# Kernel tuning notes

Measured on AMD Instinct MI355X. Metric: run time of the kernel, lower is better.

## Reference

```python
import jax, jax.numpy as jnp
import numpy as np

B, S, D, H = 4, 2048, 1024, 16
HD = D // H  # head_dim = 64


def setup_inputs() -> dict:
    key = jax.random.key(0)
    ks = jax.random.split(key, 7)
    sc = 0.02
    return {
        "data": jax.random.normal(ks[0], (B, S, D), jnp.float32),
        "context": jax.random.normal(ks[1], (B, S, D), jnp.float32),
        "Wq": jax.random.normal(ks[2], (D, D), jnp.float32) * sc,
        "bq": jnp.zeros((D,), jnp.float32),
        "Wk": jax.random.normal(ks[3], (D, D), jnp.float32) * sc,
        "bk": jnp.zeros((D,), jnp.float32),
        "Wv": jax.random.normal(ks[4], (D, D), jnp.float32) * sc,
        "bv": jnp.zeros((D,), jnp.float32),
        "Wo": jax.random.normal(ks[5], (D, D), jnp.float32) * sc,
        "bo": jnp.zeros((D,), jnp.float32),
    }


def reference(data, context, Wq, bq, Wk, bk, Wv, bv, Wo, bo):
    # Projections (torch Linear: x @ W.T + b; here W stored as [in, out])
    Q = data @ Wq + bq          # [B,S,D]
    K = context @ Wk + bk
    V = context @ Wv + bv
    # split heads -> [B,H,S,HD]
    Q = Q.reshape(B, S, H, HD).transpose(0, 2, 1, 3)
    K = K.reshape(B, S, H, HD).transpose(0, 2, 1, 3)
    V = V.reshape(B, S, H, HD).transpose(0, 2, 1, 3)
    scale = jnp.sqrt(jnp.asarray(HD, Q.dtype))
    scores = jnp.einsum("bhqd,bhkd->bhqk", Q, K) / scale  # [B,H,S,S]
    causal = jnp.tril(jnp.ones((S, S), bool))              # row >= col
    scores = jnp.where(causal[None, None], scores, jnp.asarray(-jnp.inf, scores.dtype))
    probs = jax.nn.softmax(scores, axis=-1)
    Z = jnp.einsum("bhqk,bhkd->bhqd", probs, V)            # [B,H,S,HD]
    Z = Z.transpose(0, 2, 1, 3).reshape(B, S, D)
    return Z @ Wo + bo
```

## Files before the change

kernel.cpp:

```cpp
#include <hip/hip_runtime.h>

#define B_  4
#define S_  2048
#define D_  1024
#define H_  16
#define HD_ 64
#define M_  (B_*S_)

typedef _Float16 f16;
typedef f16  f16x8 __attribute__((ext_vector_type(8)));
typedef f16  f16x4 __attribute__((ext_vector_type(4)));
typedef float f32x4 __attribute__((ext_vector_type(4)));

__device__ __forceinline__ void gload_lds16(const f16* g, f16* l) {
    __builtin_amdgcn_global_load_lds(
        (const __attribute__((address_space(1))) void*)g,
        (__attribute__((address_space(3))) void*)l, 16, 0, 0);
}

__global__ __launch_bounds__(256) void cvt2_kernel(const float* __restrict__ a,
                                                   const float* __restrict__ c,
                                                   f16* __restrict__ out, int n4each) {
    int i = blockIdx.x * 256 + threadIdx.x;
    const float* src = (i < n4each) ? a : c;
    int j = (i < n4each) ? i : i - n4each;
    f32x4 v = *reinterpret_cast<const f32x4*>(src + (size_t)j * 4);
    *reinterpret_cast<f16x4*>(out + (size_t)i * 4) = __builtin_convertvector(v, f16x4);
}

__global__ __launch_bounds__(256) void transpose_cvt4_kernel(const float* __restrict__ Wq,
                                                             const float* __restrict__ Wk,
                                                             const float* __restrict__ Wv,
                                                             const float* __restrict__ Wo,
                                                             f16* __restrict__ WT) {
    __shared__ float tile[32][33];
    const int z = blockIdx.z;
    const float* W = (z == 0) ? Wq : (z == 1) ? Wk : (z == 2) ? Wv : Wo;
    f16* dst = WT + (size_t)z * D_ * D_;
    const int n0 = blockIdx.x * 32, k0 = blockIdx.y * 32;
    const int tx = threadIdx.x & 31, ty = threadIdx.x >> 5;
#pragma unroll
    for (int j = 0; j < 4; ++j)
        tile[ty + 8 * j][tx] = W[(size_t)(k0 + ty + 8 * j) * D_ + n0 + tx];
    __syncthreads();
#pragma unroll
    for (int j = 0; j < 4; ++j)
        dst[(size_t)(n0 + ty + 8 * j) * D_ + k0 + tx] = (f16)tile[tx][ty + 8 * j];
}

__global__ __launch_bounds__(512, 2) void gemm_qkv8(const f16* __restrict__ Adata,
                                                    const f16* __restrict__ Actx,
                                                    const f16* __restrict__ Wt,
                                                    const float* __restrict__ bq,
                                                    const float* __restrict__ bk,
                                                    const float* __restrict__ bv,
                                                    f16* __restrict__ Qb,
                                                    f16* __restrict__ Kb,
                                                    f16* __restrict__ VtB) {
    extern __shared__ __align__(16) f16 SM[];
    constexpr int K = D_;
    constexpr int NT = K / 64;
    const int id = (int)(blockIdx.y * 12 + blockIdx.x);
    const int work = (id & 7) * 48 + (id >> 3);
    const int wy = work / 12, wx = work - wy * 12;
    const int seg = wx >> 2;
    const f16* __restrict__ A = seg ? Actx : Adata;
    const int m0 = wy * 256, n0 = wx * 256;
    const int tid = (int)threadIdx.x;
    const int w = tid >> 6, l = tid & 63, lr = l & 15, lg = l >> 4;
    const int wr = w >> 2, wc = w & 3;
    const int swx = lr & 7;
    const int srow = tid >> 3;
    const int g16 = (tid & 7) ^ (srow & 7);

    auto stageH = [&](int buf, int kt, int mat, int h) {
        const f16* __restrict__ src = mat ? (Wt + (size_t)(n0 + h * 128) * K)
                                          : (A + (size_t)(m0 + h * 128) * K);
        f16* dst = SM + mat * 32768 + buf * 16384 + h * 8192;
        const int kk0 = kt * 64;
        gload_lds16(src + (size_t)srow * K + kk0 + g16 * 8, dst + w * 512);
        gload_lds16(src + (size_t)(srow + 64) * K + kk0 + g16 * 8, dst + 4096 + w * 512);
    };
    auto LDA = [&](int buf, int m, int kk) -> f16x8 {
        const int gr = m * 32 + wr * 16 + lr;
        return *reinterpret_cast<const f16x8*>(
            SM + buf * 16384 + (gr >> 7) * 8192 + (gr & 127) * 64 + (((kk * 4 + lg) ^ swx) * 8));
    };
    auto LDB = [&](int buf, int n, int kk) -> f16x8 {
        const int gr = n * 64 + wc * 16 + lr;
        return *reinterpret_cast<const f16x8*>(
            SM + 32768 + buf * 16384 + (gr >> 7) * 8192 + (gr & 127) * 64 + (((kk * 4 + lg) ^ swx) * 8));
    };

    f32x4 acc[8][4] = {};
    stageH(0, 0, 0, 0); stageH(0, 0, 1, 0); stageH(0, 0, 1, 1); stageH(0, 0, 0, 1);
    asm volatile("s_waitcnt vmcnt(4)" ::: "memory");
    __builtin_amdgcn_s_barrier();

    for (int t = 0; t < NT; ++t) {
        const int buf = t & 1, nb = buf ^ 1;
        const bool nl = (t + 1 < NT);
        f16x8 a[4][2], b[4][2];
#pragma unroll
        for (int m = 0; m < 4; ++m) { a[m][0] = LDA(buf, m, 0); a[m][1] = LDA(buf, m, 1); }
#pragma unroll
        for (int n = 0; n < 2; ++n) { b[n][0] = LDB(buf, n, 0); b[n][1] = LDB(buf, n, 1); }
        if (nl) { stageH(nb, t + 1, 0, 0); asm volatile("s_waitcnt vmcnt(4)" ::: "memory"); }
        else    { asm volatile("s_waitcnt vmcnt(2)" ::: "memory"); }
        __builtin_amdgcn_s_barrier();
        __builtin_amdgcn_s_setprio(1);
#pragma unroll
        for (int kk = 0; kk < 2; ++kk)
#pragma unroll
            for (int m = 0; m < 4; ++m)
#pragma unroll
                for (int n = 0; n < 2; ++n)
                    acc[m][n] = __builtin_amdgcn_mfma_f32_16x16x32_f16(a[m][kk], b[n][kk], acc[m][n], 0, 0, 0);
        __builtin_amdgcn_s_setprio(0);
        __builtin_amdgcn_s_barrier();
#pragma unroll
        for (int n = 2; n < 4; ++n) { b[n][0] = LDB(buf, n, 0); b[n][1] = LDB(buf, n, 1); }
        if (nl) { stageH(nb, t + 1, 1, 0); asm volatile("s_waitcnt vmcnt(4)" ::: "memory"); }
        else    { asm volatile("s_waitcnt vmcnt(0)" ::: "memory"); }
        __builtin_amdgcn_s_barrier();
        __builtin_amdgcn_s_setprio(1);
#pragma unroll
        for (int kk = 0; kk < 2; ++kk)
#pragma unroll
            for (int m = 0; m < 4; ++m)
#pragma unroll
                for (int n = 2; n < 4; ++n)
                    acc[m][n] = __builtin_amdgcn_mfma_f32_16x16x32_f16(a[m][kk], b[n][kk], acc[m][n], 0, 0, 0);
        __builtin_amdgcn_s_setprio(0);
        __builtin_amdgcn_s_barrier();
#pragma unroll
        for (int m = 0; m < 4; ++m) { a[m][0] = LDA(buf, m + 4, 0); a[m][1] = LDA(buf, m + 4, 1); }
        if (nl) stageH(nb, t + 1, 1, 1);
        __builtin_amdgcn_s_barrier();
        __builtin_amdgcn_s_setprio(1);
#pragma unroll
        for (int kk = 0; kk < 2; ++kk)
#pragma unroll
            for (int m = 0; m < 4; ++m)
#pragma unroll
                for (int n = 2; n < 4; ++n)
                    acc[m + 4][n] = __builtin_amdgcn_mfma_f32_16x16x32_f16(a[m][kk], b[n][kk], acc[m + 4][n], 0, 0, 0);
        __builtin_amdgcn_s_setprio(0);
        __builtin_amdgcn_s_barrier();
        if (nl) { stageH(nb, t + 1, 0, 1); asm volatile("s_waitcnt vmcnt(4)" ::: "memory"); }
        __builtin_amdgcn_s_barrier();
        __builtin_amdgcn_s_setprio(1);
#pragma unroll
        for (int kk = 0; kk < 2; ++kk)
#pragma unroll
            for (int m = 0; m < 4; ++m)
#pragma unroll
                for (int n = 0; n < 2; ++n)
                    acc[m + 4][n] = __builtin_amdgcn_mfma_f32_16x16x32_f16(a[m][kk], b[n][kk], acc[m + 4][n], 0, 0, 0);
        __builtin_amdgcn_s_setprio(0);
        __builtin_amdgcn_s_barrier();
    }
    const float* bias = (seg == 0) ? bq : (seg == 1) ? bk : bv;
#pragma unroll
    for (int n = 0; n < 4; ++n) {
        const int col = n0 + n * 64 + wc * 16 + lr;
        const int lc = col & 1023;
        const float bvv = bias[lc];
#pragma unroll
        for (int m = 0; m < 8; ++m) {
            const int row = m0 + m * 32 + wr * 16 + lg * 4;
            if (seg == 2) {
                const int bb = row >> 11, s0 = row & 2047;
                f16x4 v;
#pragma unroll
                for (int r = 0; r < 4; ++r) v[r] = (f16)(acc[m][n][r] + bvv);
                *reinterpret_cast<f16x4*>(VtB + ((size_t)(bb * D_ + lc)) * S_ + s0) = v;
            } else {
                f16* dst = seg ? Kb : Qb;
#pragma unroll
                for (int r = 0; r < 4; ++r)
                    dst[(size_t)(row + r) * D_ + lc] = (f16)(acc[m][n][r] + bvv);
            }
        }
    }
}

__global__ __launch_bounds__(256, 2) void gemm_out3(const f16* __restrict__ A,
                                                    const f16* __restrict__ Wt,
                                                    const float* __restrict__ bias,
                                                    float* __restrict__ Cout) {
    extern __shared__ __align__(16) f16 SM[];
    constexpr int K = D_;
    constexpr int NT = K / 32;
    const int id = (int)blockIdx.x;
    const int work = (id & 7) * 32 + (id >> 3);
    const int wy = work >> 2, wx = work & 3;
    const int m0 = wy * 128, n0 = wx * 256;
    const int tid = (int)threadIdx.x;
    const int w = tid >> 6, lr = tid & 15, lg = (tid & 63) >> 4;
    const int wr = w >> 1, wc = w & 1;
    const int sw = (lr >> 1) & 3;

    auto stage = [&](int buf, int kt) {
        const int kk0 = kt * 32;
        f16* base = SM + buf * 12288;
#pragma unroll
        for (int j = 0; j < 2; ++j) {
            const int c = j * 256 + tid;
            const int row = c >> 2;
            const int ks = ((c & 3) ^ ((row >> 1) & 3)) * 8;
            gload_lds16(A + (size_t)(m0 + row) * K + kk0 + ks,
                        base + (j * 256 + w * 64) * 8);
        }
#pragma unroll
        for (int j = 0; j < 4; ++j) {
            const int c = j * 256 + tid;
            const int row = c >> 2;
            const int ks = ((c & 3) ^ ((row >> 1) & 3)) * 8;
            gload_lds16(Wt + (size_t)(n0 + row) * K + kk0 + ks,
                        base + 4096 + (j * 256 + w * 64) * 8);
        }
    };
    auto LDA = [&](int buf, int m) -> f16x8 {
        return *reinterpret_cast<const f16x8*>(
            SM + buf * 12288 + (wr * 64 + m * 16 + lr) * 32 + ((lg ^ sw) * 8));
    };
    auto LDB = [&](int buf, int n) -> f16x8 {
        return *reinterpret_cast<const f16x8*>(
            SM + buf * 12288 + 4096 + (wc * 128 + n * 16 + lr) * 32 + ((lg ^ sw) * 8));
    };

    f32x4 acc[4][8] = {};
    stage(0, 0);
    stage(1, 1);
    asm volatile("s_waitcnt vmcnt(6)" ::: "memory");
    __builtin_amdgcn_s_barrier();

    int buf = 0;
    for (int t = 0; t < NT; ++t) {
        if (t + 2 < NT) {
            int nb = buf + 2; if (nb >= 3) nb -= 3;
            stage(nb, t + 2);
        }
        f16x8 a[4], b[8];
#pragma unroll
        for (int m = 0; m < 4; ++m) a[m] = LDA(buf, m);
#pragma unroll
        for (int n = 0; n < 8; ++n) b[n] = LDB(buf, n);
        __builtin_amdgcn_s_setprio(1);
#pragma unroll
        for (int m = 0; m < 4; ++m)
#pragma unroll
            for (int n = 0; n < 8; ++n)
                acc[m][n] = __builtin_amdgcn_mfma_f32_16x16x32_f16(a[m], b[n], acc[m][n], 0, 0, 0);
        __builtin_amdgcn_s_setprio(0);
        if (t + 2 < NT) {
            asm volatile("s_waitcnt vmcnt(6)" ::: "memory");
        } else if (t + 1 < NT) {
            asm volatile("s_waitcnt vmcnt(0)" ::: "memory");
        }
        __builtin_amdgcn_s_barrier();
        if (++buf >= 3) buf = 0;
    }
#pragma unroll
    for (int n = 0; n < 8; ++n) {
        const int col = n0 + wc * 128 + n * 16 + lr;
        const float bvv = bias[col];
#pragma unroll
        for (int m = 0; m < 4; ++m) {
            const int row = m0 + wr * 64 + m * 16 + lg * 4;
#pragma unroll
            for (int r = 0; r < 4; ++r)
                Cout[(size_t)(row + r) * D_ + col] = acc[m][n][r] + bvv;
        }
    }
}

__global__ __launch_bounds__(256, 2) void attn_kernel(const f16* __restrict__ Q,
                                                      const f16* __restrict__ Kg,
                                                      const f16* __restrict__ Vt,
                                                      f16* __restrict__ Z) {
    __shared__ __align__(16) f16 KL[2][64 * 64];
    __shared__ __align__(16) f16 VL[2][64 * 64];
    __shared__ __align__(16) f16 Pl[4][32][72];
    const int h = blockIdx.x, b = blockIdx.y, pp = blockIdx.z;
    const int tid = threadIdx.x, w = tid >> 6, l = tid & 63, lr = l & 15, lg = l >> 4;
    const size_t base   = ((size_t)b * S_) * D_ + h * HD_;
    const size_t vtbase = ((size_t)(b * D_ + h * HD_)) * S_;
    const f16* __restrict__ Kbase = Kg + base;
    const f16* __restrict__ Vbase = Vt + vtbase;
    const float sc = 0.125f * 1.44269504f;
    const int sw_xor = lr & 7;
    f16x8 onesv;
#pragma unroll
    for (int i = 0; i < 8; ++i) onesv[i] = (f16)1.0f;

    auto stageKV = [&](int buf, int t0) {
#pragma unroll
        for (int i = 0; i < 2; ++i) {
            const int c = i * 256 + tid;
            const int row = c >> 3, g16 = (c & 7) ^ (row & 7);
            f16* dstK = &KL[buf][(i * 256 + w * 64) * 8];
            f16* dstV = &VL[buf][(i * 256 + w * 64) * 8];
            gload_lds16(Kbase + (size_t)(t0 + row) * D_ + g16 * 8, dstK);
            gload_lds16(Vbase + (size_t)row * S_ + t0 + g16 * 8, dstV);
        }
    };

    for (int half = 0; half < 2; ++half) {
        const int qt = half ? pp : (15 - pp);
        const int q0 = qt * 128, wq0 = q0 + w * 32;
        const int ntw = ((wq0 + 31) >> 6) + 1;
        const int ntb = qt * 2 + 2;

        f16x8 qf[2][2];
#pragma unroll
        for (int mf = 0; mf < 2; ++mf)
#pragma unroll
            for (int kd = 0; kd < 2; ++kd)
                qf[mf][kd] = *reinterpret_cast<const f16x8*>(
                    Q + base + (size_t)(wq0 + mf * 16 + lr) * D_ + kd * 32 + lg * 8);

        f32x4 zacc[2][4] = {};
        f32x4 lsv[2] = {};
        float mrun[2] = {-3.0e38f, -3.0e38f};

        stageKV(0, 0);
        for (int t = 0; t < ntb; ++t) {
            const int buf = t & 1;
            if (t + 1 < ntb) {
                stageKV(buf ^ 1, (t + 1) * 64);
                asm volatile("s_waitcnt vmcnt(4)" ::: "memory");
            } else {
                asm volatile("s_waitcnt vmcnt(0)" ::: "memory");
            }
            __builtin_amdgcn_s_barrier();
            if (t < ntw) {
                const int t0 = t * 64;
                f16x8 kf[2][4];
#pragma unroll
                for (int kd = 0; kd < 2; ++kd)
#pragma unroll
                    for (int n = 0; n < 4; ++n)
                        kf[kd][n] = *reinterpret_cast<const f16x8*>(
                            &KL[buf][(n * 16 + lr) * 64 + (((kd * 4 + lg) ^ sw_xor) * 8)]);
                f32x4 sf[2][4] = {};
                __builtin_amdgcn_s_setprio(1);
#pragma unroll
                for (int kd = 0; kd < 2; ++kd)
#pragma unroll
                    for (int n = 0; n < 4; ++n)
#pragma unroll
                        for (int mf = 0; mf < 2; ++mf)
                            sf[mf][n] = __builtin_amdgcn_mfma_f32_16x16x32_f16(kf[kd][n], qf[mf][kd], sf[mf][n], 0, 0, 0);
                __builtin_amdgcn_s_setprio(0);
                f16x8 vf[2][4];
#pragma unroll
                for (int kt = 0; kt < 2; ++kt)
#pragma unroll
                    for (int n = 0; n < 4; ++n)
                        vf[kt][n] = *reinterpret_cast<const f16x8*>(
                            &VL[buf][(n * 16 + lr) * 64 + (((kt * 4 + lg) ^ sw_xor) * 8)]);
                if (t == ntw - 1) {
#pragma unroll
                    for (int mf = 0; mf < 2; ++mf)
#pragma unroll
                        for (int n = 0; n < 4; ++n)
#pragma unroll
                            for (int r = 0; r < 4; ++r)
                                if ((t0 + n * 16 + lg * 4 + r) > (wq0 + mf * 16 + lr))
                                    sf[mf][n][r] = -3.0e38f;
                }
#pragma unroll
                for (int mf = 0; mf < 2; ++mf) {
                    f32x4 t4;
#pragma unroll
                    for (int r = 0; r < 4; ++r)
                        t4[r] = fmaxf(fmaxf(sf[mf][0][r], sf[mf][1][r]), fmaxf(sf[mf][2][r], sf[mf][3][r]));
                    float vmax = fmaxf(fmaxf(t4[0], t4[1]), fmaxf(t4[2], t4[3]));
                    vmax = fmaxf(vmax, __shfl_xor(vmax, 16));
                    vmax = fmaxf(vmax, __shfl_xor(vmax, 32));
                    const float vs = vmax * sc;
                    const bool norm = !__all(vs <= mrun[mf] + 10.0f);
                    if (norm) {
                        const float mnew = fmaxf(mrun[mf], vs);
                        const float al = __builtin_amdgcn_exp2f(mrun[mf] - mnew);
                        mrun[mf] = mnew;
#pragma unroll
                        for (int r = 0; r < 4; ++r) {
                            const float ar = __shfl(al, lg * 4 + r);
#pragma unroll
                            for (int n = 0; n < 4; ++n) zacc[mf][n][r] *= ar;
                            lsv[mf][r] *= ar;
                        }
                    }
#pragma unroll
                    for (int n = 0; n < 4; ++n) {
                        f32x4 p;
#pragma unroll
                        for (int r = 0; r < 4; ++r)
                            p[r] = __builtin_amdgcn_exp2f(fmaf(sf[mf][n][r], sc, -mrun[mf]));
                        f16x4 pv;
#pragma unroll
                        for (int r = 0; r < 4; ++r) pv[r] = (f16)p[r];
                        *reinterpret_cast<f16x4*>(&Pl[w][mf * 16 + lr][n * 16 + lg * 4]) = pv;
                    }
                }
#pragma unroll
                for (int kt = 0; kt < 2; ++kt) {
                    f16x8 pa[2];
#pragma unroll
                    for (int mf = 0; mf < 2; ++mf)
                        pa[mf] = *reinterpret_cast<const f16x8*>(&Pl[w][mf * 16 + lr][kt * 32 + lg * 8]);
                    __builtin_amdgcn_s_setprio(1);
#pragma unroll
                    for (int n = 0; n < 4; ++n)
#pragma unroll
                        for (int mf = 0; mf < 2; ++mf)
                            zacc[mf][n] = __builtin_amdgcn_mfma_f32_16x16x32_f16(pa[mf], vf[kt][n], zacc[mf][n], 0, 0, 0);
#pragma unroll
                    for (int mf = 0; mf < 2; ++mf)
                        lsv[mf] = __builtin_amdgcn_mfma_f32_16x16x32_f16(pa[mf], onesv, lsv[mf], 0, 0, 0);
                    __builtin_amdgcn_s_setprio(0);
                }
            }
            __builtin_amdgcn_s_barrier();
        }
#pragma unroll
        for (int mf = 0; mf < 2; ++mf) {
            f32x4 inv;
#pragma unroll
            for (int r = 0; r < 4; ++r) inv[r] = 1.0f / lsv[mf][r];
#pragma unroll
            for (int r = 0; r < 4; ++r)
#pragma unroll
                for (int n = 0; n < 4; ++n)
                    Z[base + (size_t)(wq0 + mf * 16 + lg * 4 + r) * D_ + n * 16 + lr] =
                        (f16)(zacc[mf][n][r] * inv[r]);
        }
    }
}

extern "C" void kernel_launch(void* const* d_in, const int* in_sizes, int n_in,
                              void* d_out, int out_size, void* d_ws, size_t ws_size,
                              hipStream_t stream) {
    const float* data    = (const float*)d_in[0];
    const float* context = (const float*)d_in[1];
    const float* Wq = (const float*)d_in[2];
    const float* bq = (const float*)d_in[3];
    const float* Wk = (const float*)d_in[4];
    const float* bk = (const float*)d_in[5];
    const float* Wv = (const float*)d_in[6];
    const float* bv = (const float*)d_in[7];
    const float* Wo = (const float*)d_in[8];
    const float* bo = (const float*)d_in[9];

    const size_t MD = (size_t)M_ * D_;
    const size_t DD = (size_t)D_ * D_;
    f16* dataB = (f16*)d_ws;
    f16* ctxB  = dataB + MD;
    f16* WqT   = ctxB + MD;
    f16* WkT   = WqT + DD;
    f16* WvT   = WkT + DD;
    f16* WoT   = WvT + DD;
    f16* Qb    = WoT + DD;
    f16* Kb    = Qb + MD;
    f16* VtB   = Kb + MD;
    f16* Zb    = VtB + MD;

    (void)WkT; (void)WvT;

    const int n4 = (int)(MD / 4);
    cvt2_kernel<<<2 * n4 / 256, 256, 0, stream>>>(data, context, dataB, n4);
    transpose_cvt4_kernel<<<dim3(32, 32, 4), 256, 0, stream>>>(Wq, Wk, Wv, Wo, WqT);

    hipFuncSetAttribute(reinterpret_cast<const void*>(gemm_qkv8),
                        hipFuncAttributeMaxDynamicSharedMemorySize, 131072);
    hipFuncSetAttribute(reinterpret_cast<const void*>(gemm_out3),
                        hipFuncAttributeMaxDynamicSharedMemorySize, 73728);

    gemm_qkv8<<<dim3(12, 32), 512, 131072, stream>>>(dataB, ctxB, WqT, bq, bk, bv,
                                                     Qb, Kb, VtB);

    attn_kernel<<<dim3(H_, B_, 8), 256, 0, stream>>>(Qb, Kb, VtB, Zb);

    gemm_out3<<<256, 256, 73728, stream>>>(Zb, WoT, bo, (float*)d_out);
}
```

Measured before the change: 174.7 us.

## Deepen QKV GEMM prefetch pipeline to stage tiles two iterations ahead

Restructures the projection GEMM main loop so global-to-LDS loads for tile t+2 are issued into the current buffer partway through tile t, with a prologue preloading most of tile 1. Waits become explicit vmcnt thresholds per phase, and the last two iterations are peeled with their own wait counts. The fourth MFMA phase is merged into the third, which removes one barrier pair per tile. The goal is to hide more global memory latency behind MFMA work. The tighter buffer reuse and hand-tuned vmcnt values risk races or stalls if the counts are wrong.

After: 176.1 us. No clear change (+0.8%).

```diff
diff --git a/kernel.cpp b/kernel.cpp
--- a/kernel.cpp
+++ b/kernel.cpp
@@ -16,6 +16,15 @@
     __builtin_amdgcn_global_load_lds(
         (const __attribute__((address_space(1))) void*)g,
         (__attribute__((address_space(3))) void*)l, 16, 0, 0);
+}
+
+__device__ __forceinline__ void vmwait(int n) {
+    if (n < 0) return;
+    else if (n == 0)  asm volatile("s_waitcnt vmcnt(0)" ::: "memory");
+    else if (n == 2)  asm volatile("s_waitcnt vmcnt(2)" ::: "memory");
+    else if (n == 4)  asm volatile("s_waitcnt vmcnt(4)" ::: "memory");
+    else if (n == 8)  asm volatile("s_waitcnt vmcnt(8)" ::: "memory");
+    else              asm volatile("s_waitcnt vmcnt(10)" ::: "memory");
 }
 
 __global__ __launch_bounds__(256) void cvt2_kernel(const float* __restrict__ a,
@@ -93,20 +102,26 @@
     };
 
     f32x4 acc[8][4] = {};
-    stageH(0, 0, 0, 0); stageH(0, 0, 1, 0); stageH(0, 0, 1, 1); stageH(0, 0, 0, 1);
-    asm volatile("s_waitcnt vmcnt(4)" ::: "memory");
+
+    stageH(0, 0, 0, 0);
+    stageH(0, 0, 1, 0);
+    stageH(0, 0, 1, 1);
+    stageH(0, 0, 0, 1);
+    stageH(1, 1, 0, 0);
+    stageH(1, 1, 1, 0);
+    stageH(1, 1, 1, 1);
+    vmwait(10);
     __builtin_amdgcn_s_barrier();
 
-    for (int t = 0; t < NT; ++t) {
+    auto tile = [&](int t, int w1, int w2, int w3, bool stg1, bool stg2) {
         const int buf = t & 1, nb = buf ^ 1;
-        const bool nl = (t + 1 < NT);
         f16x8 a[4][2], b[4][2];
 #pragma unroll
         for (int m = 0; m < 4; ++m) { a[m][0] = LDA(buf, m, 0); a[m][1] = LDA(buf, m, 1); }
 #pragma unroll
         for (int n = 0; n < 2; ++n) { b[n][0] = LDB(buf, n, 0); b[n][1] = LDB(buf, n, 1); }
-        if (nl) { stageH(nb, t + 1, 0, 0); asm volatile("s_waitcnt vmcnt(4)" ::: "memory"); }
-        else    { asm volatile("s_waitcnt vmcnt(2)" ::: "memory"); }
+        if (stg1) stageH(nb, t + 1, 0, 1);
+        vmwait(w1);
         __builtin_amdgcn_s_barrier();
         __builtin_amdgcn_s_setprio(1);
 #pragma unroll
@@ -120,8 +135,8 @@
         __builtin_amdgcn_s_barrier();
 #pragma unroll
         for (int n = 2; n < 4; ++n) { b[n][0] = LDB(buf, n, 0); b[n][1] = LDB(buf, n, 1); }
-        if (nl) { stageH(nb, t + 1, 1, 0); asm volatile("s_waitcnt vmcnt(4)" ::: "memory"); }
-        else    { asm volatile("s_waitcnt vmcnt(0)" ::: "memory"); }
+        if (stg2) stageH(buf, t + 2, 0, 0);
+        vmwait(w2);
         __builtin_amdgcn_s_barrier();
         __builtin_amdgcn_s_setprio(1);
 #pragma unroll
@@ -135,7 +150,8 @@
         __builtin_amdgcn_s_barrier();
 #pragma unroll
         for (int m = 0; m < 4; ++m) { a[m][0] = LDA(buf, m + 4, 0); a[m][1] = LDA(buf, m + 4, 1); }
-        if (nl) stageH(nb, t + 1, 1, 1);
+        if (stg2) { stageH(buf, t + 2, 1, 0); stageH(buf, t + 2, 1, 1); }
+        vmwait(w3);
         __builtin_amdgcn_s_barrier();
         __builtin_amdgcn_s_setprio(1);
 #pragma unroll
@@ -143,23 +159,16 @@
 #pragma unroll
             for (int m = 0; m < 4; ++m)
 #pragma unroll
-                for (int n = 2; n < 4; ++n)
+                for (int n = 0; n < 4; ++n)
                     acc[m + 4][n] = __builtin_amdgcn_mfma_f32_16x16x32_f16(a[m][kk], b[n][kk], acc[m + 4][n], 0, 0, 0);
         __builtin_amdgcn_s_setprio(0);
         __builtin_amdgcn_s_barrier();
-        if (nl) { stageH(nb, t + 1, 0, 1); asm volatile("s_waitcnt vmcnt(4)" ::: "memory"); }
-        __builtin_amdgcn_s_barrier();
-        __builtin_amdgcn_s_setprio(1);
-#pragma unroll
-        for (int kk = 0; kk < 2; ++kk)
-#pragma unroll
-            for (int m = 0; m < 4; ++m)
-#pragma unroll
-                for (int n = 0; n < 2; ++n)
-                    acc[m + 4][n] = __builtin_amdgcn_mfma_f32_16x16x32_f16(a[m][kk], b[n][kk], acc[m + 4][n], 0, 0, 0);
-        __builtin_amdgcn_s_setprio(0);
-        __builtin_amdgcn_s_barrier();
-    }
+    };
+
+    for (int t = 0; t < NT - 2; ++t) tile(t, 10, 10, 10, true, true);
+    tile(NT - 2, 10, 8, 4, true, false);
+    tile(NT - 1, 2, 0, -1, false, false);
+
     const float* bias = (seg == 0) ? bq : (seg == 1) ? bk : bv;
 #pragma unroll
     for (int n = 0; n < 4; ++n) {
```
